# Performance work log

Hardware: AMD Instinct MI355X
Metric: run time of the kernel (lower is better)

Reference implementation:

```python
import jax, jax.numpy as jnp
import numpy as np

N_NODES = 50000
N_EDGES = 800000
IN_F, HID_F, OUT_F = 256, 128, 64
NEG_SLOPE = 0.2
EPS = 1e-16


def _aggregate_with_attention(x, src, tgt, a_w, a_b, num_nodes):
    # x: [N, d]; src/tgt: [E]; a_w: [2d]; a_b: [1]
    d = x.shape[-1]
    x_src = x[src]                                   # [E, d] gather
    # att(cat([x_src, x_tgt])) == x_src @ a_w[:d] + x_tgt @ a_w[d:] + b
    alpha = x_src @ a_w[:d] + x[tgt] @ a_w[d:] + a_b[0]   # [E]
    alpha = jnp.where(alpha >= 0, alpha, NEG_SLOPE * alpha)  # leaky_relu(0.2)
    # segment softmax over edges grouped by target node
    m = jax.ops.segment_max(alpha, tgt, num_segments=num_nodes)   # [N]
    e = jnp.exp(alpha - m[tgt])                                    # [E]
    s = jax.ops.segment_sum(e, tgt, num_segments=num_nodes)       # [N]
    alpha = e / (s[tgt] + EPS)                                     # [E]
    msgs = x_src * alpha[:, None]                                  # [E, d]
    return jax.ops.segment_sum(msgs, tgt, num_segments=num_nodes)  # [N, d]


def setup_inputs() -> dict:
    key = jax.random.key(0)
    ks = jax.random.split(key, 10)
    x = jax.random.normal(ks[0], (N_NODES, IN_F), dtype=jnp.float32)
    edge_index = jax.random.randint(ks[1], (2, N_EDGES), 0, N_NODES, dtype=jnp.int32)
    sc1 = 1.0 / np.sqrt(IN_F)
    sc2 = 1.0 / np.sqrt(HID_F)
    return {
        "x": x,
        "edge_index": edge_index,
        "W1": jax.random.normal(ks[2], (IN_F, HID_F), dtype=jnp.float32) * sc1,
        "b1": jax.random.normal(ks[3], (HID_F,), dtype=jnp.float32) * sc1,
        "a1_w": jax.random.normal(ks[4], (2 * HID_F,), dtype=jnp.float32) * sc2,
        "a1_b": jax.random.normal(ks[5], (1,), dtype=jnp.float32) * sc2,
        "W2": jax.random.normal(ks[6], (HID_F, OUT_F), dtype=jnp.float32) * sc2,
        "b2": jax.random.normal(ks[7], (OUT_F,), dtype=jnp.float32) * sc2,
        "a2_w": jax.random.normal(ks[8], (2 * OUT_F,), dtype=jnp.float32) * (1.0 / np.sqrt(OUT_F)),
        "a2_b": jax.random.normal(ks[9], (1,), dtype=jnp.float32) * (1.0 / np.sqrt(OUT_F)),
    }


def reference(x, edge_index, W1, b1, a1_w, a1_b, W2, b2, a2_w, a2_b):
    src, tgt = edge_index[0], edge_index[1]
    n = x.shape[0]
    # eval mode: dropout is identity
    h = jax.nn.elu(x @ W1 + b1)                           # [N, HID]
    h = _aggregate_with_attention(h, src, tgt, a1_w, a1_b, n)
    o = h @ W2 + b2                                        # [N, OUT]
    o = _aggregate_with_attention(o, src, tgt, a2_w, a2_b, n)
    return jax.nn.log_softmax(o, axis=-1)
```

## Files before the change

kernel.cpp:

```cpp
#include <hip/hip_runtime.h>

#define NN    50000
#define NE    800000
#define INF_  256
#define HIDF  128
#define OUTF  64
#define NBUCK 196
#define CAP   5120
#define CHUNK 2048
#define NPART1 ((NE + CHUNK - 1) / CHUNK)
#define NLIN1  ((NN + 63) / 64)
#define NPREP  160

typedef unsigned int uint;
typedef unsigned short ushort;
typedef __attribute__((ext_vector_type(8))) short short8;
typedef __attribute__((ext_vector_type(4))) float float4v;

__device__ __forceinline__ short f2bf(float f) {
    union { float f; unsigned u; } v; v.f = f;
    unsigned r = v.u + 0x7fffu + ((v.u >> 16) & 1u);
    return (short)(r >> 16);
}
__device__ __forceinline__ float bflo(uint u) {
    union { uint u; float f; } v; v.u = u << 16; return v.f;
}
__device__ __forceinline__ float bfhi(uint u) {
    union { uint u; float f; } v; v.u = u & 0xffff0000u; return v.f;
}

__device__ __forceinline__ int excl_scan256(int v, int* ws) {
    int lane = threadIdx.x & 63, wv = threadIdx.x >> 6;
    int x = v;
    #pragma unroll
    for (int o = 1; o < 64; o <<= 1) {
        int y = __shfl_up(x, o);
        if (lane >= o) x += y;
    }
    if (lane == 63) ws[wv] = x;
    __syncthreads();
    int add = 0;
    #pragma unroll
    for (int w = 0; w < 4; w++) add += (w < wv) ? ws[w] : 0;
    return x + add - v;
}

__global__ __launch_bounds__(256) void k_prep(const float* __restrict__ W1, const float* __restrict__ W2,
                                              short* __restrict__ W1f, short* __restrict__ W2f,
                                              int* __restrict__ bcur) {
    if (blockIdx.x == NPREP) {
        if (threadIdx.x < NBUCK) bcur[threadIdx.x] = 0;
        return;
    }
    int i = blockIdx.x * 256 + threadIdx.x;
    if (i < INF_ * HIDF) {
        int kk = i & 7, t = i >> 3;
        int m_l = t & 15, q = (t >> 4) & 3, s = t >> 6;
        int nb = s & 7, kc = s >> 3;
        int k = kc * 32 + q * 8 + kk, n = nb * 16 + m_l;
        W1f[i] = f2bf(W1[k * HIDF + n]);
    } else if (i < INF_ * HIDF + HIDF * OUTF) {
        int i2 = i - INF_ * HIDF;
        int kk = i2 & 7, t = i2 >> 3;
        int m_l = t & 15, q = (t >> 4) & 3, s = t >> 6;
        int nb = s & 3, kc = s >> 2;
        int k = kc * 32 + q * 8 + kk, n = nb * 16 + m_l;
        W2f[i2] = f2bf(W2[k * OUTF + n]);
    }
}


__global__ __launch_bounds__(256, 3) void k_f1(const int* __restrict__ src, const int* __restrict__ tgt,
                                               int* __restrict__ bcur, uint2* __restrict__ pairs,
                                               const float* __restrict__ X, const short* __restrict__ W1f,
                                               const float* __restrict__ b1, ushort* __restrict__ Hb,
                                               const float* __restrict__ a1w, float* __restrict__ s1s,
                                               float* __restrict__ s1t) {
    if (blockIdx.x < NPART1) {
        __shared__ int hist[NBUCK], lofs[NBUCK], cur[NBUCK], gstart[NBUCK];
        __shared__ int ws[4];
        __shared__ int ltgt[CHUNK], lsrc[CHUNK];
        int tid = threadIdx.x;
        for (int i = tid; i < NBUCK; i += 256) hist[i] = 0;
        __syncthreads();

        int base = blockIdx.x * CHUNK;
        int cnt = NE - base; if (cnt > CHUNK) cnt = CHUNK;

        int t_[8], s_[8];
        #pragma unroll
        for (int k = 0; k < 8; k++) {
            int idx = k * 256 + tid;
            if (idx < cnt) {
                int j = base + idx;
                t_[k] = tgt[j]; s_[k] = src[j];
                atomicAdd(&hist[t_[k] >> 8], 1);
            } else t_[k] = -1;
        }
        __syncthreads();

        int v = (tid < NBUCK) ? hist[tid] : 0;
        int excl = excl_scan256(v, ws);
        if (tid < NBUCK) {
            lofs[tid] = excl;
            cur[tid] = excl;
            gstart[tid] = atomicAdd(&bcur[tid], v);
        }
        __syncthreads();

        #pragma unroll
        for (int k = 0; k < 8; k++) {
            if (t_[k] >= 0) {
                int b = t_[k] >> 8;
                int pos = atomicAdd(&cur[b], 1);
                ltgt[pos] = t_[k]; lsrc[pos] = s_[k];
            }
        }
        __syncthreads();

        for (int j = tid; j < cnt; j += 256) {
            int tv = ltgt[j];
            int b = tv >> 8;
            int dst = gstart[b] + (j - lofs[b]);
            pairs[(size_t)b * CAP + dst] = make_uint2((uint)tv, (uint)lsrc[j]);
        }
        return;
    }
    int bid = blockIdx.x - NPART1;
    int w = threadIdx.x >> 6;
    int l = threadIdx.x & 63;
    int m_l = l & 15, q = l >> 4;
    int row0 = bid * 64 + w * 16;
    int rA0 = row0 + m_l;
    int rc0 = rA0 < NN ? rA0 : NN - 1;
    const float* pa0 = X + (size_t)rc0 * INF_ + q * 8;
    const short8* Bp = (const short8*)W1f;

    float4v acc[8] = {};
    #pragma unroll
    for (int kc = 0; kc < 8; kc++) {
        int k0 = kc * 32;
        float4 u0 = *(const float4*)(pa0 + k0);
        float4 u1 = *(const float4*)(pa0 + k0 + 4);
        short8 a0;
        a0[0] = f2bf(u0.x); a0[1] = f2bf(u0.y); a0[2] = f2bf(u0.z); a0[3] = f2bf(u0.w);
        a0[4] = f2bf(u1.x); a0[5] = f2bf(u1.y); a0[6] = f2bf(u1.z); a0[7] = f2bf(u1.w);
        #pragma unroll
        for (int n = 0; n < 8; n++) {
            short8 b = Bp[(kc * 8 + n) * 64 + l];
            acc[n] = __builtin_amdgcn_mfma_f32_16x16x32_bf16(a0, b, acc[n], 0, 0, 0);
        }
    }

    float vs_r[4] = {0.f, 0.f, 0.f, 0.f}, vt_r[4] = {0.f, 0.f, 0.f, 0.f};
    #pragma unroll
    for (int n = 0; n < 8; n++) {
        int col = n * 16 + m_l;
        float bias = b1[col];
        float aw0 = a1w[col], aw1 = a1w[HIDF + col];
        #pragma unroll
        for (int r = 0; r < 4; r++) {
            int row = row0 + q * 4 + r;
            float v = acc[n][r] + bias;
            v = v > 0.f ? v : expm1f(v);
            vs_r[r] += v * aw0; vt_r[r] += v * aw1;
            if (row < NN) Hb[(size_t)row * HIDF + col] = (ushort)f2bf(v);
        }
    }
    #pragma unroll
    for (int r = 0; r < 4; r++) {
        #pragma unroll
        for (int o = 1; o < 16; o <<= 1) {
            vs_r[r] += __shfl_xor(vs_r[r], o);
            vt_r[r] += __shfl_xor(vt_r[r], o);
        }
    }
    if (m_l == 0) {
        #pragma unroll
        for (int r = 0; r < 4; r++) {
            int row = row0 + q * 4 + r;
            if (row < NN) { s1s[row] = vs_r[r]; s1t[row] = vt_r[r]; }
        }
    }
}

__global__ __launch_bounds__(256) void k_part2(const int* __restrict__ bcur, const uint2* __restrict__ pairs,
                                               int* __restrict__ fsrc, int* __restrict__ nbeg,
                                               int* __restrict__ ncnt) {
    __shared__ int hist[256], cur[256];
    __shared__ int ws[4];
    int tid = threadIdx.x;
    int b = blockIdx.x;
    int cnt = __builtin_amdgcn_readfirstlane(bcur[b]);
    hist[tid] = 0;
    __syncthreads();

    const uint2* pb = pairs + (size_t)b * CAP;
    for (int j = tid; j < cnt; j += 256) {
        uint2 e = pb[j];
        atomicAdd(&hist[e.x & 255], 1);
    }
    __syncthreads();

    int v = hist[tid];
    int excl = excl_scan256(v, ws);
    int node = (b << 8) + tid;
    if (node < NN) { nbeg[node] = b * CAP + excl; ncnt[node] = v; }
    cur[tid] = excl;
    __syncthreads();

    for (int j = tid; j < cnt; j += 256) {
        uint2 e = pb[j];
        int pos = atomicAdd(&cur[e.x & 255], 1);
        fsrc[(size_t)b * CAP + pos] = (int)e.y;
    }
}

__global__ __launch_bounds__(256, 3) void k_linear2(const short* __restrict__ Hin, const short* __restrict__ W2f,
                                                    const float* __restrict__ b2, ushort* __restrict__ Ob,
                                                    const float* __restrict__ a2w, float* __restrict__ s2s,
                                                    float* __restrict__ s2t) {
    int w = threadIdx.x >> 6;
    int l = threadIdx.x & 63;
    int m_l = l & 15, q = l >> 4;
    int row0 = blockIdx.x * 64 + w * 16;
    int rA0 = row0 + m_l;
    int rc0 = rA0 < NN ? rA0 : NN - 1;
    const short* pa0 = Hin + (size_t)rc0 * HIDF + q * 8;
    const short8* Bp = (const short8*)W2f;

    float4v acc[4] = {};
    #pragma unroll
    for (int kc = 0; kc < 4; kc++) {
        int k0 = kc * 32;
        short8 a0 = *(const short8*)(pa0 + k0);
        #pragma unroll
        for (int n = 0; n < 4; n++) {
            short8 b = Bp[(kc * 4 + n) * 64 + l];
            acc[n] = __builtin_amdgcn_mfma_f32_16x16x32_bf16(a0, b, acc[n], 0, 0, 0);
        }
    }

    float vs_r[4] = {0.f, 0.f, 0.f, 0.f}, vt_r[4] = {0.f, 0.f, 0.f, 0.f};
    #pragma unroll
    for (int n = 0; n < 4; n++) {
        int col = n * 16 + m_l;
        float bias = b2[col];
        float aw0 = a2w[col], aw1 = a2w[OUTF + col];
        #pragma unroll
        for (int r = 0; r < 4; r++) {
            int row = row0 + q * 4 + r;
            float v = acc[n][r] + bias;
            vs_r[r] += v * aw0; vt_r[r] += v * aw1;
            if (row < NN) Ob[(size_t)row * OUTF + col] = (ushort)f2bf(v);
        }
    }
    #pragma unroll
    for (int r = 0; r < 4; r++) {
        #pragma unroll
        for (int o = 1; o < 16; o <<= 1) {
            vs_r[r] += __shfl_xor(vs_r[r], o);
            vt_r[r] += __shfl_xor(vt_r[r], o);
        }
    }
    if (m_l == 0) {
        #pragma unroll
        for (int r = 0; r < 4; r++) {
            int row = row0 + q * 4 + r;
            if (row < NN) { s2s[row] = vs_r[r]; s2t[row] = vt_r[r]; }
        }
    }
}


__global__ __launch_bounds__(256) void k_agg1f(const uint* __restrict__ Hb4, const int* __restrict__ nbeg,
                                               const int* __restrict__ ncnt, const int* __restrict__ fsrc,
                                               const float* __restrict__ ss, const float* __restrict__ st_,
                                               const float* __restrict__ ab, uint* __restrict__ Hagg4) {
    int wid  = (blockIdx.x * 256 + threadIdx.x) >> 6;
    int lane = threadIdx.x & 63;
    if (wid >= NN) return;
    int beg = __builtin_amdgcn_readfirstlane(nbeg[wid]);
    int deg = __builtin_amdgcn_readfirstlane(ncnt[wid]);
    int end = beg + deg;
    float bias = ab[0] + st_[wid];
    float ax = 0.f, ay = 0.f, bx = 0.f, by = 0.f;

    if (deg > 0 && deg <= 64) {
        int my_s = 0; float a = -INFINITY;
        if (lane < deg) {
            my_s = fsrc[beg + lane];
            float t = ss[my_s] + bias;
            a = t >= 0.f ? t : 0.2f * t;
        }
        float m = a;
        #pragma unroll
        for (int o = 32; o > 0; o >>= 1) m = fmaxf(m, __shfl_xor(m, o));
        float e = (lane < deg) ? __expf(a - m) : 0.f;
        float sum = e;
        #pragma unroll
        for (int o = 32; o > 0; o >>= 1) sum += __shfl_xor(sum, o);
        float p = e * (1.f / (sum + 1e-16f));
        for (int j = 0; j < deg; j += 8) {
            int sA[8]; float wA[8]; uint xA[8];
            #pragma unroll
            for (int u = 0; u < 8; u++) { sA[u] = __shfl(my_s, j + u); wA[u] = __shfl(p, j + u); }
            #pragma unroll
            for (int u = 0; u < 8; u++) xA[u] = Hb4[(size_t)sA[u] * 64 + lane];
            #pragma unroll
            for (int u = 0; u < 8; u += 2) {
                ax += wA[u] * bflo(xA[u]);     ay += wA[u] * bfhi(xA[u]);
                bx += wA[u + 1] * bflo(xA[u + 1]); by += wA[u + 1] * bfhi(xA[u + 1]);
            }
        }
    } else if (deg > 64) {
        float m = -INFINITY;
        for (int i = beg + lane; i < end; i += 64) {
            float t = ss[fsrc[i]] + bias;
            t = t >= 0.f ? t : 0.2f * t;
            m = fmaxf(m, t);
        }
        #pragma unroll
        for (int o = 32; o > 0; o >>= 1) m = fmaxf(m, __shfl_xor(m, o));
        float sum = 0.f;
        for (int i = beg + lane; i < end; i += 64) {
            float t = ss[fsrc[i]] + bias;
            t = t >= 0.f ? t : 0.2f * t;
            sum += __expf(t - m);
        }
        #pragma unroll
        for (int o = 32; o > 0; o >>= 1) sum += __shfl_xor(sum, o);
        float inv = 1.f / (sum + 1e-16f);
        for (int c = beg; c < end; c += 64) {
            int cnt = min(64, end - c);
            int my_s = 0; float p = 0.f;
            if (lane < cnt) {
                my_s = fsrc[c + lane];
                float t = ss[my_s] + bias;
                t = t >= 0.f ? t : 0.2f * t;
                p = __expf(t - m) * inv;
            }
            for (int j = 0; j < cnt; j += 4) {
                int s0 = __shfl(my_s, j),     s1 = __shfl(my_s, j + 1);
                int s2 = __shfl(my_s, j + 2), s3 = __shfl(my_s, j + 3);
                float w0 = __shfl(p, j),     w1 = __shfl(p, j + 1);
                float w2 = __shfl(p, j + 2), w3 = __shfl(p, j + 3);
                uint x0 = Hb4[(size_t)s0 * 64 + lane];
                uint x1 = Hb4[(size_t)s1 * 64 + lane];
                uint x2 = Hb4[(size_t)s2 * 64 + lane];
                uint x3 = Hb4[(size_t)s3 * 64 + lane];
                ax += w0 * bflo(x0); ay += w0 * bfhi(x0);
                bx += w1 * bflo(x1); by += w1 * bfhi(x1);
                ax += w2 * bflo(x2); ay += w2 * bfhi(x2);
                bx += w3 * bflo(x3); by += w3 * bfhi(x3);
            }
        }
    }
    float fx = ax + bx, fy = ay + by;
    uint outv = (uint)(ushort)f2bf(fx) | ((uint)(ushort)f2bf(fy) << 16);
    Hagg4[(size_t)wid * 64 + lane] = outv;
}

__global__ __launch_bounds__(256) void k_agg2f(const uint* __restrict__ Ob4, const int* __restrict__ nbeg,
                                               const int* __restrict__ ncnt, const int* __restrict__ fsrc,
                                               const float* __restrict__ ss, const float* __restrict__ st_,
                                               const float* __restrict__ ab, float* __restrict__ out) {
    int wid  = (blockIdx.x * 256 + threadIdx.x) >> 6;
    int lane = threadIdx.x & 63;
    if (wid >= NN) return;
    int half = lane >> 5, li = lane & 31;
    int beg = __builtin_amdgcn_readfirstlane(nbeg[wid]);
    int deg = __builtin_amdgcn_readfirstlane(ncnt[wid]);
    int end = beg + deg;
    float bias = ab[0] + st_[wid];
    float a0 = 0.f, a1 = 0.f;

    if (deg > 0 && deg <= 64) {
        int my_s = 0; float a = -INFINITY;
        if (lane < deg) {
            my_s = fsrc[beg + lane];
            float t = ss[my_s] + bias;
            a = t >= 0.f ? t : 0.2f * t;
        }
        float m = a;
        #pragma unroll
        for (int o = 32; o > 0; o >>= 1) m = fmaxf(m, __shfl_xor(m, o));
        float e = (lane < deg) ? __expf(a - m) : 0.f;
        float sum = e;
        #pragma unroll
        for (int o = 32; o > 0; o >>= 1) sum += __shfl_xor(sum, o);
        float p = e * (1.f / (sum + 1e-16f));
        for (int j = 0; j < deg; j += 8) {
            int e0 = j + half, e1 = j + 2 + half, e2 = j + 4 + half, e3 = j + 6 + half;
            int s0 = __shfl(my_s, e0), s1 = __shfl(my_s, e1);
            int s2 = __shfl(my_s, e2), s3 = __shfl(my_s, e3);
            float w0 = __shfl(p, e0), w1 = __shfl(p, e1);
            float w2 = __shfl(p, e2), w3 = __shfl(p, e3);
            uint x0 = Ob4[(size_t)s0 * 32 + li];
            uint x1 = Ob4[(size_t)s1 * 32 + li];
            uint x2 = Ob4[(size_t)s2 * 32 + li];
            uint x3 = Ob4[(size_t)s3 * 32 + li];
            a0 += w0 * bflo(x0); a1 += w0 * bfhi(x0);
            a0 += w1 * bflo(x1); a1 += w1 * bfhi(x1);
            a0 += w2 * bflo(x2); a1 += w2 * bfhi(x2);
            a0 += w3 * bflo(x3); a1 += w3 * bfhi(x3);
        }
    } else if (deg > 64) {
        float m = -INFINITY;
        for (int i = beg + lane; i < end; i += 64) {
            float t = ss[fsrc[i]] + bias;
            t = t >= 0.f ? t : 0.2f * t;
            m = fmaxf(m, t);
        }
        #pragma unroll
        for (int o = 32; o > 0; o >>= 1) m = fmaxf(m, __shfl_xor(m, o));
        float sum = 0.f;
        for (int i = beg + lane; i < end; i += 64) {
            float t = ss[fsrc[i]] + bias;
            t = t >= 0.f ? t : 0.2f * t;
            sum += __expf(t - m);
        }
        #pragma unroll
        for (int o = 32; o > 0; o >>= 1) sum += __shfl_xor(sum, o);
        float inv = 1.f / (sum + 1e-16f);
        for (int c = beg; c < end; c += 64) {
            int cnt = min(64, end - c);
            int my_s = 0; float p = 0.f;
            if (lane < cnt) {
                my_s = fsrc[c + lane];
                float t = ss[my_s] + bias;
                t = t >= 0.f ? t : 0.2f * t;
                p = __expf(t - m) * inv;
            }
            for (int j = 0; j < cnt; j += 4) {
                int e0 = j + half, e1 = j + 2 + half;
                int s0 = __shfl(my_s, e0), s1 = __shfl(my_s, e1);
                float w0 = __shfl(p, e0), w1 = __shfl(p, e1);
                uint x0 = Ob4[(size_t)s0 * 32 + li];
                uint x1 = Ob4[(size_t)s1 * 32 + li];
                a0 += w0 * bflo(x0); a1 += w0 * bfhi(x0);
                a0 += w1 * bflo(x1); a1 += w1 * bfhi(x1);
            }
        }
    }
    a0 += __shfl_xor(a0, 32);
    a1 += __shfl_xor(a1, 32);
    float mx = fmaxf(a0, a1);
    #pragma unroll
    for (int o = 16; o > 0; o >>= 1) mx = fmaxf(mx, __shfl_xor(mx, o));
    float es = __expf(a0 - mx) + __expf(a1 - mx);
    #pragma unroll
    for (int o = 16; o > 0; o >>= 1) es += __shfl_xor(es, o);
    float lg = __logf(es);
    if (half == 0) {
        float2 r; r.x = a0 - mx - lg; r.y = a1 - mx - lg;
        ((float2*)out)[(size_t)wid * 32 + li] = r;
    }
}


extern "C" void kernel_launch(void* const* d_in, const int* in_sizes, int n_in,
                              void* d_out, int out_size, void* d_ws, size_t ws_size,
                              hipStream_t stream) {
    const float* X   = (const float*)d_in[0];
    const int*   ei  = (const int*)d_in[1];
    const float* W1  = (const float*)d_in[2];
    const float* b1  = (const float*)d_in[3];
    const float* a1w = (const float*)d_in[4];
    const float* a1b = (const float*)d_in[5];
    const float* W2  = (const float*)d_in[6];
    const float* b2  = (const float*)d_in[7];
    const float* a2w = (const float*)d_in[8];
    const float* a2b = (const float*)d_in[9];
    const int* src = ei;
    const int* tgt = ei + NE;

    char* p = (char*)d_ws;
    size_t off = 0;
    auto alloc = [&](size_t bytes) -> char* {
        char* r = p + off;
        off = (off + bytes + 255) & ~(size_t)255;
        return r;
    };
    ushort* Hb    = (ushort*)alloc((size_t)NN * HIDF * 2);
    ushort* Hagg  = (ushort*)alloc((size_t)NN * HIDF * 2);
    ushort* Ob    = (ushort*)alloc((size_t)NN * OUTF * 2);
    short* W1f    = (short*)alloc((size_t)INF_ * HIDF * 2);
    short* W2f    = (short*)alloc((size_t)HIDF * OUTF * 2);
    float* s1s    = (float*)alloc((size_t)NN * 4);
    float* s1t    = (float*)alloc((size_t)NN * 4);
    float* s2s    = (float*)alloc((size_t)NN * 4);
    float* s2t    = (float*)alloc((size_t)NN * 4);
    int*   bcur   = (int*)alloc((size_t)NBUCK * 4);
    uint2* pairs  = (uint2*)alloc((size_t)NBUCK * CAP * 8);
    int*   fsrc   = (int*)alloc((size_t)NBUCK * CAP * 4);
    int*   nbeg   = (int*)alloc((size_t)NN * 4);
    int*   ncnt   = (int*)alloc((size_t)NN * 4);

    k_prep   <<<NPREP + 1, 256, 0, stream>>>(W1, W2, W1f, W2f, bcur);
    k_f1     <<<NPART1 + NLIN1, 256, 0, stream>>>(src, tgt, bcur, pairs,
                                                  X, W1f, b1, Hb, a1w, s1s, s1t);
    k_part2  <<<NBUCK, 256, 0, stream>>>(bcur, pairs, fsrc, nbeg, ncnt);
    k_agg1f  <<<NN / 4, 256, 0, stream>>>((const uint*)Hb, nbeg, ncnt, fsrc, s1s, s1t, a1b, (uint*)Hagg);
    k_linear2<<<NLIN1, 256, 0, stream>>>((const short*)Hagg, W2f, b2, Ob, a2w, s2s, s2t);
    k_agg2f  <<<NN / 4, 256, 0, stream>>>((const uint*)Ob, nbeg, ncnt, fsrc, s2s, s2t, a2b, (float*)d_out);
}
```

Before: 212.5 us.

## Fuse second linear layer into layer-1 aggregation kernel and prefetch X loads

Removes the separate k_linear2 launch and the Hagg intermediate. Each wave, after aggregating a node's 128-dim hidden vector, now computes the 64-wide W2 projection with shuffles and scalar FMAs against a repacked bf16 W2, and writes Ob plus the attention scores s2s and s2t directly. This saves a global write and read of the aggregated hidden features and one launch, but replaces MFMA work with per-lane FMA and shuffle loops inside the aggregation kernel. Separately, k_f1 now loads all X chunks before converting them and issuing MFMAs, which adds latency overlap at the cost of more registers.

```diff
diff --git a/kernel.cpp b/kernel.cpp
--- a/kernel.cpp
+++ b/kernel.cpp
@@ -10,7 +10,7 @@
 #define CHUNK 2048
 #define NPART1 ((NE + CHUNK - 1) / CHUNK)
 #define NLIN1  ((NN + 63) / 64)
-#define NPREP  160
+#define NPREP  144
 
 typedef unsigned int uint;
 typedef unsigned short ushort;
@@ -46,7 +46,7 @@
 }
 
 __global__ __launch_bounds__(256) void k_prep(const float* __restrict__ W1, const float* __restrict__ W2,
-                                              short* __restrict__ W1f, short* __restrict__ W2f,
+                                              short* __restrict__ W1f, uint* __restrict__ W2i,
                                               int* __restrict__ bcur) {
     if (blockIdx.x == NPREP) {
         if (threadIdx.x < NBUCK) bcur[threadIdx.x] = 0;
@@ -59,13 +59,12 @@
         int nb = s & 7, kc = s >> 3;
         int k = kc * 32 + q * 8 + kk, n = nb * 16 + m_l;
         W1f[i] = f2bf(W1[k * HIDF + n]);
-    } else if (i < INF_ * HIDF + HIDF * OUTF) {
+    } else {
         int i2 = i - INF_ * HIDF;
-        int kk = i2 & 7, t = i2 >> 3;
-        int m_l = t & 15, q = (t >> 4) & 3, s = t >> 6;
-        int nb = s & 3, kc = s >> 2;
-        int k = kc * 32 + q * 8 + kk, n = nb * 16 + m_l;
-        W2f[i2] = f2bf(W2[k * OUTF + n]);
+        int l = i2 >> 6, c = i2 & 63;
+        uint pk = (uint)(ushort)f2bf(W2[(2 * l) * OUTF + c]) |
+                  ((uint)(ushort)f2bf(W2[(2 * l + 1) * OUTF + c]) << 16);
+        W2i[i2] = pk;
     }
 }
 
@@ -136,19 +135,27 @@
     const float* pa0 = X + (size_t)rc0 * INF_ + q * 8;
     const short8* Bp = (const short8*)W1f;
 
+    float4 xu[16];
+    #pragma unroll
+    for (int kc = 0; kc < 8; kc++) {
+        xu[2 * kc]     = *(const float4*)(pa0 + kc * 32);
+        xu[2 * kc + 1] = *(const float4*)(pa0 + kc * 32 + 4);
+    }
+    short8 af[8];
+    #pragma unroll
+    for (int kc = 0; kc < 8; kc++) {
+        float4 u0 = xu[2 * kc], u1 = xu[2 * kc + 1];
+        af[kc][0] = f2bf(u0.x); af[kc][1] = f2bf(u0.y); af[kc][2] = f2bf(u0.z); af[kc][3] = f2bf(u0.w);
+        af[kc][4] = f2bf(u1.x); af[kc][5] = f2bf(u1.y); af[kc][6] = f2bf(u1.z); af[kc][7] = f2bf(u1.w);
+    }
+
     float4v acc[8] = {};
     #pragma unroll
     for (int kc = 0; kc < 8; kc++) {
-        int k0 = kc * 32;
-        float4 u0 = *(const float4*)(pa0 + k0);
-        float4 u1 = *(const float4*)(pa0 + k0 + 4);
-        short8 a0;
-        a0[0] = f2bf(u0.x); a0[1] = f2bf(u0.y); a0[2] = f2bf(u0.z); a0[3] = f2bf(u0.w);
-        a0[4] = f2bf(u1.x); a0[5] = f2bf(u1.y); a0[6] = f2bf(u1.z); a0[7] = f2bf(u1.w);
         #pragma unroll
         for (int n = 0; n < 8; n++) {
             short8 b = Bp[(kc * 8 + n) * 64 + l];
-            acc[n] = __builtin_amdgcn_mfma_f32_16x16x32_bf16(a0, b, acc[n], 0, 0, 0);
+            acc[n] = __builtin_amdgcn_mfma_f32_16x16x32_bf16(af[kc], b, acc[n], 0, 0, 0);
         }
     }
 
@@ -216,67 +223,14 @@
     }
 }
 
-__global__ __launch_bounds__(256, 3) void k_linear2(const short* __restrict__ Hin, const short* __restrict__ W2f,
-                                                    const float* __restrict__ b2, ushort* __restrict__ Ob,
-                                                    const float* __restrict__ a2w, float* __restrict__ s2s,
-                                                    float* __restrict__ s2t) {
-    int w = threadIdx.x >> 6;
-    int l = threadIdx.x & 63;
-    int m_l = l & 15, q = l >> 4;
-    int row0 = blockIdx.x * 64 + w * 16;
-    int rA0 = row0 + m_l;
-    int rc0 = rA0 < NN ? rA0 : NN - 1;
-    const short* pa0 = Hin + (size_t)rc0 * HIDF + q * 8;
-    const short8* Bp = (const short8*)W2f;
-
-    float4v acc[4] = {};
-    #pragma unroll
-    for (int kc = 0; kc < 4; kc++) {
-        int k0 = kc * 32;
-        short8 a0 = *(const short8*)(pa0 + k0);
-        #pragma unroll
-        for (int n = 0; n < 4; n++) {
-            short8 b = Bp[(kc * 4 + n) * 64 + l];
-            acc[n] = __builtin_amdgcn_mfma_f32_16x16x32_bf16(a0, b, acc[n], 0, 0, 0);
-        }
-    }
-
-    float vs_r[4] = {0.f, 0.f, 0.f, 0.f}, vt_r[4] = {0.f, 0.f, 0.f, 0.f};
-    #pragma unroll
-    for (int n = 0; n < 4; n++) {
-        int col = n * 16 + m_l;
-        float bias = b2[col];
-        float aw0 = a2w[col], aw1 = a2w[OUTF + col];
-        #pragma unroll
-        for (int r = 0; r < 4; r++) {
-            int row = row0 + q * 4 + r;
-            float v = acc[n][r] + bias;
-            vs_r[r] += v * aw0; vt_r[r] += v * aw1;
-            if (row < NN) Ob[(size_t)row * OUTF + col] = (ushort)f2bf(v);
-        }
-    }
-    #pragma unroll
-    for (int r = 0; r < 4; r++) {
-        #pragma unroll
-        for (int o = 1; o < 16; o <<= 1) {
-            vs_r[r] += __shfl_xor(vs_r[r], o);
-            vt_r[r] += __shfl_xor(vt_r[r], o);
-        }
-    }
-    if (m_l == 0) {
-        #pragma unroll
-        for (int r = 0; r < 4; r++) {
-            int row = row0 + q * 4 + r;
-            if (row < NN) { s2s[row] = vs_r[r]; s2t[row] = vt_r[r]; }
-        }
-    }
-}
-
-
-__global__ __launch_bounds__(256) void k_agg1f(const uint* __restrict__ Hb4, const int* __restrict__ nbeg,
-                                               const int* __restrict__ ncnt, const int* __restrict__ fsrc,
-                                               const float* __restrict__ ss, const float* __restrict__ st_,
-                                               const float* __restrict__ ab, uint* __restrict__ Hagg4) {
+
+__global__ __launch_bounds__(256) void k_agg1l2(const uint* __restrict__ Hb4, const int* __restrict__ nbeg,
+                                                const int* __restrict__ ncnt, const int* __restrict__ fsrc,
+                                                const float* __restrict__ ss, const float* __restrict__ st_,
+                                                const float* __restrict__ ab, const uint* __restrict__ W2i,
+                                                const float* __restrict__ b2, const float* __restrict__ a2w,
+                                                uint* __restrict__ Ob4, float* __restrict__ s2s,
+                                                float* __restrict__ s2t) {
     int wid  = (blockIdx.x * 256 + threadIdx.x) >> 6;
     int lane = threadIdx.x & 63;
     if (wid >= NN) return;
@@ -309,7 +263,7 @@
             for (int u = 0; u < 8; u++) xA[u] = Hb4[(size_t)sA[u] * 64 + lane];
             #pragma unroll
             for (int u = 0; u < 8; u += 2) {
-                ax += wA[u] * bflo(xA[u]);     ay += wA[u] * bfhi(xA[u]);
+                ax += wA[u] * bflo(xA[u]);         ay += wA[u] * bfhi(xA[u]);
                 bx += wA[u + 1] * bflo(xA[u + 1]); by += wA[u + 1] * bfhi(xA[u + 1]);
             }
         }
@@ -357,8 +311,31 @@
         }
     }
     float fx = ax + bx, fy = ay + by;
-    uint outv = (uint)(ushort)f2bf(fx) | ((uint)(ushort)f2bf(fy) << 16);
-    Hagg4[(size_t)wid * 64 + lane] = outv;
+
+    float oc = b2[lane];
+    #pragma unroll 2
+    for (int l0 = 0; l0 < 64; l0 += 8) {
+        uint wv[8];
+        #pragma unroll
+        for (int u = 0; u < 8; u++) wv[u] = W2i[(l0 + u) * 64 + lane];
+        #pragma unroll
+        for (int u = 0; u < 8; u++) {
+            float h0 = __shfl(fx, l0 + u);
+            float h1 = __shfl(fy, l0 + u);
+            oc += h0 * bflo(wv[u]) + h1 * bfhi(wv[u]);
+        }
+    }
+
+    float vs = oc * a2w[lane];
+    float vt = oc * a2w[OUTF + lane];
+    #pragma unroll
+    for (int o = 32; o > 0; o >>= 1) { vs += __shfl_xor(vs, o); vt += __shfl_xor(vt, o); }
+    if (lane == 0) { s2s[wid] = vs; s2t[wid] = vt; }
+
+    int li = lane & 31;
+    float e0 = __shfl(oc, li * 2), e1 = __shfl(oc, li * 2 + 1);
+    uint pk = (uint)(ushort)f2bf(e0) | ((uint)(ushort)f2bf(e1) << 16);
+    if (lane < 32) Ob4[(size_t)wid * 32 + li] = pk;
 }
 
 __global__ __launch_bounds__(256) void k_agg2f(const uint* __restrict__ Ob4, const int* __restrict__ nbeg,
@@ -483,10 +460,9 @@
         return r;
     };
     ushort* Hb    = (ushort*)alloc((size_t)NN * HIDF * 2);
-    ushort* Hagg  = (ushort*)alloc((size_t)NN * HIDF * 2);
     ushort* Ob    = (ushort*)alloc((size_t)NN * OUTF * 2);
     short* W1f    = (short*)alloc((size_t)INF_ * HIDF * 2);
-    short* W2f    = (short*)alloc((size_t)HIDF * OUTF * 2);
+    uint*  W2i    = (uint*)alloc((size_t)(HIDF / 2) * OUTF * 4);
     float* s1s    = (float*)alloc((size_t)NN * 4);
     float* s1t    = (float*)alloc((size_t)NN * 4);
     float* s2s    = (float*)alloc((size_t)NN * 4);
@@ -497,11 +473,11 @@
     int*   nbeg   = (int*)alloc((size_t)NN * 4);
     int*   ncnt   = (int*)alloc((size_t)NN * 4);
 
-    k_prep   <<<NPREP + 1, 256, 0, stream>>>(W1, W2, W1f, W2f, bcur);
-    k_f1     <<<NPART1 + NLIN1, 256, 0, stream>>>(src, tgt, bcur, pairs,
-                                                  X, W1f, b1, Hb, a1w, s1s, s1t);
-    k_part2  <<<NBUCK, 256, 0, stream>>>(bcur, pairs, fsrc, nbeg, ncnt);
-    k_agg1f  <<<NN / 4, 256, 0, stream>>>((const uint*)Hb, nbeg, ncnt, fsrc, s1s, s1t, a1b, (uint*)Hagg);
-    k_linear2<<<NLIN1, 256, 0, stream>>>((const short*)Hagg, W2f, b2, Ob, a2w, s2s, s2t);
-    k_agg2f  <<<NN / 4, 256, 0, stream>>>((const uint*)Ob, nbeg, ncnt, fsrc, s2s, s2t, a2b, (float*)d_out);
-}
+    k_prep  <<<NPREP + 1, 256, 0, stream>>>(W1, W2, W1f, W2i, bcur);
+    k_f1    <<<NPART1 + NLIN1, 256, 0, stream>>>(src, tgt, bcur, pairs,
+                                                 X, W1f, b1, Hb, a1w, s1s, s1t);
+    k_part2 <<<NBUCK, 256, 0, stream>>>(bcur, pairs, fsrc, nbeg, ncnt);
+    k_agg1l2<<<NN / 4, 256, 0, stream>>>((const uint*)Hb, nbeg, ncnt, fsrc, s1s, s1t, a1b,
+                                         W2i, b2, a2w, (uint*)Ob, s2s, s2t);
+    k_agg2f <<<NN / 4, 256, 0, stream>>>((const uint*)Ob, nbeg, ncnt, fsrc, s2s, s2t, a2b, (float*)d_out);
+}
```

Result: slower. 272.5 us (+28.2%).
